# Performance work log

Hardware: AMD Instinct MI355X
Metric: run time of the kernel (lower is better)

Reference implementation:

```python
import jax, jax.numpy as jnp
import numpy as np

BLOCKS = 16
TEMP = 0.7
SINK_ITERS = 8
CUT = 8
GUMBEL_EPS = 1e-6
IN_EPS = 1e-5
NEG = -1e9  # stands in for log(0) = -inf; exp(NEG) == 0 in fp32, avoids nan grads


def setup_inputs() -> dict:
    key = jax.random.key(0)
    k1, k2, k3 = jax.random.split(key, 3)
    shape = (8, 512, 4096, 1)  # [B, C, H, W=1]
    return {
        "q": jax.random.normal(k1, shape, jnp.float32),
        "k": jax.random.normal(k2, shape, jnp.float32),
        "v": jax.random.normal(k3, shape, jnp.float32),
    }


def _block_cat(x, blocks):
    # torch: cat(x.chunk(blocks, dim=2)[:-1], dim=-1)
    # [B,C,H,W] -> [B,C,H/blocks,(blocks-1)*W]
    B, C, H, W = x.shape
    Hb = H // blocks
    xb = x.reshape(B, C, blocks, Hb, W)[:, :, : blocks - 1]  # drop last chunk
    return jnp.transpose(xb, (0, 1, 3, 2, 4)).reshape(B, C, Hb, (blocks - 1) * W)


def reference(q, k, v):
    B, C, H, W = q.shape
    Hb = H // BLOCKS
    N = BLOCKS - 1  # number of retained blocks

    b_q = _block_cat(q, BLOCKS)  # [B,C,Hb,N]
    b_k = _block_cat(k, BLOCKS)
    b_v = _block_cat(v, BLOCKS)

    # ---- AttentionPermMatrix: Gumbel-Sinkhorn soft permutation [B,N,N] ----
    sq = jnp.swapaxes(b_q.mean(axis=1), 1, 2)  # [B,N,Hb]
    sk = jnp.swapaxes(b_k.mean(axis=1), 1, 2)
    R = jnp.einsum('bie,bje->bij', sq, sk) * (C ** -0.5)  # [B,N,N]
    Rp = jax.nn.relu(R)
    pos = R > 0
    r = jnp.where(pos, jnp.log(jnp.where(pos, Rp, 1.0)), NEG)  # safe log(relu(R))
    u = jax.random.uniform(jax.random.key(42), r.shape, r.dtype)
    gumbel = -jnp.log(-jnp.log(u + GUMBEL_EPS) + GUMBEL_EPS)
    r = (r + gumbel) / TEMP
    for _ in range(SINK_ITERS):
        r = r - jax.nn.logsumexp(r, axis=2, keepdims=True)
        r = r - jax.nn.logsumexp(r, axis=1, keepdims=True)
    perm = jnp.exp(r)  # [B,N,N]

    # ---- permute blocks of k/v (perm broadcast over channel dim C) ----
    k_sort = jnp.einsum('bchn,bnm->bchm', b_k, perm)  # [B,C,Hb,N]
    v_sort = jnp.einsum('bchn,bnm->bchm', b_v, perm)

    # ---- cut: first CUT size-1 chunks along last dim, cat along dim=-2, transpose(1,3)
    def cut(x):
        # [B,C,Hb,N] -> [B,C,CUT*Hb,1] (chunk j occupies rows j*Hb:(j+1)*Hb) -> [B,1,CUT*Hb,C]
        xc = jnp.transpose(x[..., :CUT], (0, 1, 3, 2)).reshape(B, C, CUT * Hb, 1)
        return jnp.transpose(xc, (0, 3, 2, 1))

    k_cut = cut(k_sort)  # [B,1,M,C], M = CUT*Hb
    v_cut = cut(v_sort)
    q_t = jnp.transpose(q, (0, 3, 2, 1))  # [B,1,H,C]

    logits = jnp.einsum('bwhc,bwmc->bwhm', q_t, k_cut) / TEMP  # [B,1,H,M]
    attn = jax.nn.softmax(logits, axis=-1)
    val = jnp.einsum('bwhm,bwmc->bwhc', attn, v_cut)  # [B,1,H,C]

    # InstanceNorm2d (affine=False): normalize over spatial dims (2,3) per (B, channel)
    mu = val.mean(axis=(2, 3), keepdims=True)
    var = val.var(axis=(2, 3), keepdims=True)
    return (val - mu) / jnp.sqrt(var + IN_EPS)
```

## Files before the change

kernel.cpp:

```cpp
#include <hip/hip_runtime.h>
#include <stdint.h>

typedef _Float16 half_t;
typedef _Float16 half4 __attribute__((ext_vector_type(4)));
typedef _Float16 half8 __attribute__((ext_vector_type(8)));
typedef float floatx4 __attribute__((ext_vector_type(4)));

#define B_ 8
#define C_ 512
#define H_ 4096
#define HB 256
#define NB 15
#define CUT_ 8
#define M_ 2048
#define INV_TEMP (1.0f/0.7f)
#define NEG (-1e9f)

#define KROW 528
#define KT_BYTES 33792u
#define VT_BYTES 32768u

#define SQ_OFFB   0u
#define SK_OFFB   122880u
#define ST_OFFB   245760u
#define PERM_OFFB 245824u
#define KC16_OFFB 262144u
#define VC16_OFFB (262144u + 17301504u)
#define WS_NEED   (262144u + 17301504u + 16777216u)

__device__ __forceinline__ unsigned rotl32(unsigned x, unsigned n) {
    return (x << n) | (x >> (32u - n));
}
__device__ __forceinline__ void threefry2x32(unsigned k0, unsigned k1,
                                             unsigned x0, unsigned x1,
                                             unsigned &o0, unsigned &o1) {
    unsigned k2 = 0x1BD11BDAu ^ k0 ^ k1;
    x0 += k0; x1 += k1;
    x0+=x1; x1=rotl32(x1,13); x1^=x0;
    x0+=x1; x1=rotl32(x1,15); x1^=x0;
    x0+=x1; x1=rotl32(x1,26); x1^=x0;
    x0+=x1; x1=rotl32(x1, 6); x1^=x0;
    x0+=k1; x1+=k2+1u;
    x0+=x1; x1=rotl32(x1,17); x1^=x0;
    x0+=x1; x1=rotl32(x1,29); x1^=x0;
    x0+=x1; x1=rotl32(x1,16); x1^=x0;
    x0+=x1; x1=rotl32(x1,24); x1^=x0;
    x0+=k2; x1+=k0+2u;
    x0+=x1; x1=rotl32(x1,13); x1^=x0;
    x0+=x1; x1=rotl32(x1,15); x1^=x0;
    x0+=x1; x1=rotl32(x1,26); x1^=x0;
    x0+=x1; x1=rotl32(x1, 6); x1^=x0;
    x0+=k0; x1+=k1+3u;
    x0+=x1; x1=rotl32(x1,17); x1^=x0;
    x0+=x1; x1=rotl32(x1,29); x1^=x0;
    x0+=x1; x1=rotl32(x1,16); x1^=x0;
    x0+=x1; x1=rotl32(x1,24); x1^=x0;
    x0+=k1; x1+=k2+4u;
    x0+=x1; x1=rotl32(x1,13); x1^=x0;
    x0+=x1; x1=rotl32(x1,15); x1^=x0;
    x0+=x1; x1=rotl32(x1,26); x1^=x0;
    x0+=x1; x1=rotl32(x1, 6); x1^=x0;
    x0+=k2; x1+=k0+5u;
    o0 = x0; o1 = x1;
}

__device__ __forceinline__ void stage_tile8(const char* gsrc, char* lbase,
                                            int w, int lane, int nchunk) {
    #pragma unroll
    for (int i = 0; i < 5; i++) {
        int cc = w + 8*i;
        if (cc < nchunk) {
            __builtin_amdgcn_global_load_lds(
                (const __attribute__((address_space(1))) void*)(uintptr_t)
                    (gsrc + (size_t)cc*1024u + (size_t)lane*16u),
                (__attribute__((address_space(3))) void*)(uintptr_t)
                    (lbase + (size_t)cc*1024u),
                16, 0, 0);
        }
    }
}

__global__ void colmean_kernel(const float* __restrict__ q, const float* __restrict__ k,
                               float* __restrict__ sq, float* __restrict__ sk) {
    int id  = blockIdx.x * 256 + threadIdx.x;
    int h   = id % 3840;
    int rest= id / 3840;
    int b   = rest % 8;
    int seg = rest / 8;
    int c0  = seg * 64;
    const float* qb = q + ((size_t)b*C_ + c0) * H_ + h;
    const float* kb = k + ((size_t)b*C_ + c0) * H_ + h;
    float aq = 0.f, ak = 0.f;
    #pragma unroll 8
    for (int c = 0; c < 64; c++) {
        aq += qb[(size_t)c * H_];
        ak += kb[(size_t)c * H_];
    }
    atomicAdd(&sq[b*3840 + h], aq * (1.0f/512.0f));
    atomicAdd(&sk[b*3840 + h], ak * (1.0f/512.0f));
}

__global__ void perm_kernel(const float* __restrict__ sqg, const float* __restrict__ skg,
                            float* __restrict__ perm) {
    int b = blockIdx.x;
    int tid = threadIdx.x;
    __shared__ float sqs[NB*HB];
    __shared__ float sks[NB*HB];
    __shared__ float mat[NB][16];
    __shared__ float lse[NB];
    for (int i = tid; i < NB*HB; i += 256) {
        sqs[i] = sqg[b*3840 + i];
        sks[i] = skg[b*3840 + i];
    }
    __syncthreads();
    int i = tid / 15, j = tid % 15;
    if (tid < 225) {
        float acc = 0.f;
        for (int h = 0; h < HB; h++) acc += sqs[i*HB + h] * sks[j*HB + h];
        float R = acc * 0.044194173824159216f;
        float r0 = (R > 0.0f) ? logf(R) : NEG;
        int g = (b*15 + i)*15 + j;
        unsigned o0, o1;
        threefry2x32(0u, 42u, 0u, (unsigned)g, o0, o1);
        unsigned bits = o0 ^ o1;
        float u = __uint_as_float((bits >> 9) | 0x3f800000u) - 1.0f;
        float gum = -logf(-logf(u + 1e-6f) + 1e-6f);
        mat[i][j] = (r0 + gum) * INV_TEMP;
    }
    __syncthreads();
    for (int it = 0; it < 8; it++) {
        if (tid < 15) {
            float m = -3.4e38f;
            for (int jj = 0; jj < 15; jj++) m = fmaxf(m, mat[tid][jj]);
            float s = 0.f;
            for (int jj = 0; jj < 15; jj++) s += expf(mat[tid][jj] - m);
            lse[tid] = m + logf(s);
        }
        __syncthreads();
        if (tid < 225) mat[i][j] -= lse[i];
        __syncthreads();
        if (tid < 15) {
            float m = -3.4e38f;
            for (int ii = 0; ii < 15; ii++) m = fmaxf(m, mat[ii][tid]);
            float s = 0.f;
            for (int ii = 0; ii < 15; ii++) s += expf(mat[ii][tid] - m);
            lse[tid] = m + logf(s);
        }
        __syncthreads();
        if (tid < 225) mat[i][j] -= lse[j];
        __syncthreads();
    }
    if (tid < 225) perm[b*225 + tid] = expf(mat[i][j]);
}

__global__ __launch_bounds__(256)
void kcut_kernel(const float* __restrict__ k, const float* __restrict__ perm,
                 half_t* __restrict__ kc) {
    int bid  = blockIdx.x;
    int ct   = bid & 7;
    int chalf= (bid >> 3) & 1;
    int hch  = (bid >> 4) & 7;
    int b    = bid >> 7;
    int h0 = hch * 32;
    int tid = threadIdx.x;
    __shared__ float kt[32*481];
    __shared__ float pl[NB][CUT_];
    if (tid < NB*CUT_) pl[tid/CUT_][tid%CUT_] = perm[b*225 + (tid/CUT_)*15 + (tid%CUT_)];
    int cp = tid & 31;
    int hg = tid >> 5;
    int c0 = chalf*256 + ct*32;
    for (int it = 0; it < 15; it++) {
        int slot = tid + it*256;
        int h4 = slot & 7;
        int n  = (slot >> 3) % 15;
        int cc = slot / 120;
        float4 vv = *(const float4*)&k[((size_t)(b*C_ + c0 + cc))*H_ + n*HB + h0 + h4*4];
        *(float4*)&kt[cc*481 + n*32 + h4*4] = vv;
    }
    __syncthreads();
    float acc[CUT_][4];
    #pragma unroll
    for (int j = 0; j < CUT_; j++) { acc[j][0]=0.f; acc[j][1]=0.f; acc[j][2]=0.f; acc[j][3]=0.f; }
    #pragma unroll
    for (int n = 0; n < NB; n++) {
        float kv0 = kt[cp*481 + n*32 + hg*4 + 0];
        float kv1 = kt[cp*481 + n*32 + hg*4 + 1];
        float kv2 = kt[cp*481 + n*32 + hg*4 + 2];
        float kv3 = kt[cp*481 + n*32 + hg*4 + 3];
        #pragma unroll
        for (int j = 0; j < CUT_; j++) {
            float p = pl[n][j];
            acc[j][0] += kv0*p; acc[j][1] += kv1*p; acc[j][2] += kv2*p; acc[j][3] += kv3*p;
        }
    }
    int cs = c0 + (cp ^ (8*(hg & 3)));
    #pragma unroll
    for (int j = 0; j < CUT_; j++)
        for (int q2 = 0; q2 < 4; q2++) {
            int m = j*HB + h0 + hg*4 + q2;
            kc[(((size_t)b*64 + (m>>5))*32 + (m&31))*KROW + cs] = (half_t)acc[j][q2];
        }
}

__global__ __launch_bounds__(256)
void vcut_kernel(const float* __restrict__ v, const float* __restrict__ perm,
                 half_t* __restrict__ vc) {
    int bc = blockIdx.x;
    int b = bc >> 9;
    int c = bc & 511;
    int h = threadIdx.x;
    __shared__ float pl[NB][CUT_];
    if (h < NB*CUT_) pl[h/CUT_][h%CUT_] = perm[b*225 + (h/CUT_)*15 + (h%CUT_)];
    __syncthreads();
    const float* vb = v + (size_t)bc * H_ + h;
    float av[CUT_] = {0,0,0,0,0,0,0,0};
    #pragma unroll
    for (int n = 0; n < NB; n++) {
        float vv = vb[n*HB];
        #pragma unroll
        for (int j = 0; j < CUT_; j++) av[j] += vv * pl[n][j];
    }
    #pragma unroll
    for (int j = 0; j < CUT_; j++)
        vc[(((size_t)b*64 + j*8 + (h>>5))*512 + c)*32 + (h&31)] = (half_t)av[j];
}

__global__ __launch_bounds__(512, 2)
void attn_kernel(const float* __restrict__ q, const half_t* __restrict__ kc,
                 const half_t* __restrict__ vc, float* __restrict__ out,
                 float* __restrict__ stats) {
    __shared__ half_t ktile[2][32][KROW];
    __shared__ float  spart[2][64][36];
    __shared__ half_t pslab[2][64][40];
    __shared__ float  redbuf[8][2];

    int bid = blockIdx.x;
    int b   = bid & 7;
    int h0  = (bid >> 3) * 64;
    int tid = threadIdx.x;
    int w    = tid >> 6;
    int lane = tid & 63;
    int lm   = lane & 15;
    int quad = lane >> 4;
    int wm = w & 3;
    int wc = w >> 2;
    int row = 16*wm + lm;
    int key0 = 4*quad;
    int sxk = 8*((lm >> 2) & 3);

    const char* kbytes = (const char*)kc + (size_t)b * 64u * KT_BYTES;
    const char* vbytes = (const char*)vc + (size_t)b * 64u * VT_BYTES;

    stage_tile8(kbytes, (char*)&ktile[0][0][0], w, lane, 33);

    float (*qstage)[68] = reinterpret_cast<float(*)[68]>(&spart[0][0][0]);

    half8 qhi[8], qlo[8];
    for (int ch = 0; ch < 8; ch++) {
        int c0 = ch * 64;
        asm volatile("s_waitcnt lgkmcnt(0)\n\ts_barrier" ::: "memory");
        #pragma unroll
        for (int it = 0; it < 2; it++) {
            int slot = tid + it*512;
            int cc = slot >> 4;
            int h4 = slot & 15;
            float4 qv = *(const float4*)&q[((size_t)(b*C_ + c0 + cc))*H_ + h0 + h4*4];
            qstage[h4*4+0][cc] = qv.x;
            qstage[h4*4+1][cc] = qv.y;
            qstage[h4*4+2][cc] = qv.z;
            qstage[h4*4+3][cc] = qv.w;
        }
        asm volatile("s_waitcnt lgkmcnt(0)\n\ts_barrier" ::: "memory");
        if ((ch >> 2) == wc) {
            #pragma unroll
            for (int kk = 0; kk < 2; kk++) {
                int kb = (ch & 3)*2 + kk;
                const float* qp = &qstage[row][kk*32 + quad*8];
                float4 a = *(const float4*)qp;
                float4 c4 = *(const float4*)(qp + 4);
                float vals[8] = {a.x,a.y,a.z,a.w,c4.x,c4.y,c4.z,c4.w};
                half8 hh, hl;
                #pragma unroll
                for (int j = 0; j < 8; j++) {
                    float xv = vals[j] * INV_TEMP;
                    half_t h1 = (half_t)xv;
                    hh[j] = h1;
                    hl[j] = (half_t)(xv - (float)h1);
                }
                qhi[kb] = hh; qlo[kb] = hl;
            }
        }
    }

    floatx4 O[16];
    #pragma unroll
    for (int n = 0; n < 16; n++) O[n] = (floatx4)0.f;
    floatx4 Ol = (floatx4)0.f;
    float ms = -3.4e38f;
    half8 vone;
    #pragma unroll
    for (int j = 0; j < 8; j++) vone[j] = (half_t)1.0f;

    int buf = 0;
    for (int t = 0; t < 64; t++) {
        __syncthreads();
        half8 vreg[16];
        {
            const half_t* vt = (const half_t*)(vbytes + (size_t)t*VT_BYTES);
            #pragma unroll
            for (int n = 0; n < 16; n++)
                vreg[n] = *(const half8*)(vt + (256*wc + 16*n + lm)*32 + quad*8);
        }
        if (t + 1 < 64)
            stage_tile8(kbytes + (size_t)(t+1)*KT_BYTES, (char*)&ktile[buf^1][0][0], w, lane, 33);

        floatx4 acc0 = (floatx4)0.f, acc1 = (floatx4)0.f;
        __builtin_amdgcn_s_setprio(1);
        #pragma unroll
        for (int kb = 0; kb < 8; kb++) {
            int coff = (256*wc + 32*kb + quad*8) ^ sxk;
            half8 a0 = *(const half8*)&ktile[buf][lm][coff];
            half8 a1 = *(const half8*)&ktile[buf][16 + lm][coff];
            acc0 = __builtin_amdgcn_mfma_f32_16x16x32_f16(a0, qhi[kb], acc0, 0, 0, 0);
            acc0 = __builtin_amdgcn_mfma_f32_16x16x32_f16(a0, qlo[kb], acc0, 0, 0, 0);
            acc1 = __builtin_amdgcn_mfma_f32_16x16x32_f16(a1, qhi[kb], acc1, 0, 0, 0);
            acc1 = __builtin_amdgcn_mfma_f32_16x16x32_f16(a1, qlo[kb], acc1, 0, 0, 0);
        }
        __builtin_amdgcn_s_setprio(0);
        *(floatx4*)&spart[wc][row][key0]      = acc0;
        *(floatx4*)&spart[wc][row][16 + key0] = acc1;
        asm volatile("s_waitcnt lgkmcnt(0)\n\ts_barrier" ::: "memory");

        floatx4 pp0 = *(const floatx4*)&spart[wc^1][row][key0];
        floatx4 pp1 = *(const floatx4*)&spart[wc^1][row][16 + key0];
        float s0[4], s1[4];
        #pragma unroll
        for (int r = 0; r < 4; r++) {
            s0[r] = acc0[r] + pp0[r];
            s1[r] = acc1[r] + pp1[r];
        }
        float m2 = fmaxf(fmaxf(fmaxf(s0[0],s0[1]), fmaxf(s0[2],s0[3])),
                         fmaxf(fmaxf(s1[0],s1[1]), fmaxf(s1[2],s1[3])));
        m2 = fmaxf(m2, __shfl_xor(m2, 16, 64));
        m2 = fmaxf(m2, __shfl_xor(m2, 32, 64));
        int need = (m2 > ms + 8.0f) ? 1 : 0;
        if (__any(need)) {
            float mn = fmaxf(ms, m2);
            float aown = __expf(ms - mn);
            ms = mn;
            float ar[4];
            #pragma unroll
            for (int r = 0; r < 4; r++) ar[r] = __shfl(aown, key0 + r, 64);
            #pragma unroll
            for (int r = 0; r < 4; r++) Ol[r] *= ar[r];
            #pragma unroll
            for (int n = 0; n < 16; n++) {
                #pragma unroll
                for (int r = 0; r < 4; r++) O[n][r] *= ar[r];
            }
        }
        half4 hp0, hp1;
        #pragma unroll
        for (int r = 0; r < 4; r++) {
            hp0[r] = (half_t)__expf(s0[r] - ms);
            hp1[r] = (half_t)__expf(s1[r] - ms);
        }
        *(half4*)&pslab[wc][row][key0]      = hp0;
        *(half4*)&pslab[wc][row][16 + key0] = hp1;
        half8 pa = *(const half8*)&pslab[wc][row][quad*8];
        __builtin_amdgcn_s_setprio(1);
        #pragma unroll
        for (int n = 0; n < 16; n++)
            O[n] = __builtin_amdgcn_mfma_f32_16x16x32_f16(pa, vreg[n], O[n], 0, 0, 0);
        Ol = __builtin_amdgcn_mfma_f32_16x16x32_f16(pa, vone, Ol, 0, 0, 0);
        __builtin_amdgcn_s_setprio(0);
        buf ^= 1;
    }

    float inv4[4];
    #pragma unroll
    for (int r = 0; r < 4; r++) inv4[r] = 1.0f / Ol[r];
    float sa = 0.f, sb = 0.f;
    int rowg = h0 + 16*wm + quad*4;
    #pragma unroll
    for (int n = 0; n < 16; n++) {
        #pragma unroll
        for (int r = 0; r < 4; r++) {
            float o = O[n][r] * inv4[r];
            out[((size_t)b*H_ + rowg + r)*C_ + 256*wc + 16*n + lm] = o;
            sa += o; sb += o*o;
        }
    }
    #pragma unroll
    for (int msk = 1; msk < 64; msk <<= 1) {
        sa += __shfl_xor(sa, msk, 64);
        sb += __shfl_xor(sb, msk, 64);
    }
    if (lane == 0) { redbuf[w][0] = sa; redbuf[w][1] = sb; }
    __syncthreads();
    if (tid == 0) {
        float a = 0.f, c2 = 0.f;
        for (int w2 = 0; w2 < 8; w2++) { a += redbuf[w2][0]; c2 += redbuf[w2][1]; }
        atomicAdd(&stats[b*2    ], a);
        atomicAdd(&stats[b*2 + 1], c2);
    }
}

__global__ void norm_kernel(float* __restrict__ out, const float* __restrict__ stats) {
    size_t i = (size_t)blockIdx.x * 256 + threadIdx.x;
    int b = (int)(i >> 19);
    float4 vv = ((float4*)out)[i];
    const float inv = 1.0f / (4096.0f * 512.0f);
    float mu  = stats[b*2] * inv;
    float var = stats[b*2 + 1] * inv - mu*mu;
    float rs  = rsqrtf(var + 1e-5f);
    vv.x = (vv.x - mu) * rs;
    vv.y = (vv.y - mu) * rs;
    vv.z = (vv.z - mu) * rs;
    vv.w = (vv.w - mu) * rs;
    ((float4*)out)[i] = vv;
}

extern "C" void kernel_launch(void* const* d_in, const int* in_sizes, int n_in,
                              void* d_out, int out_size, void* d_ws, size_t ws_size,
                              hipStream_t stream) {
    const float* q = (const float*)d_in[0];
    const float* k = (const float*)d_in[1];
    const float* v = (const float*)d_in[2];
    float* out = (float*)d_out;
    if (ws_size < (size_t)WS_NEED) return;

    float*  sq    = (float*) ((char*)d_ws + SQ_OFFB);
    float*  sk    = (float*) ((char*)d_ws + SK_OFFB);
    float*  stats = (float*) ((char*)d_ws + ST_OFFB);
    float*  perm  = (float*) ((char*)d_ws + PERM_OFFB);
    half_t* kc    = (half_t*)((char*)d_ws + KC16_OFFB);
    half_t* vc    = (half_t*)((char*)d_ws + VC16_OFFB);

    hipMemsetAsync(d_ws, 0, (size_t)KC16_OFFB, stream);

    colmean_kernel<<<960,  256, 0, stream>>>(q, k, sq, sk);
    perm_kernel   <<<8,    256, 0, stream>>>(sq, sk, perm);
    kcut_kernel   <<<1024, 256, 0, stream>>>(k, perm, kc);
    vcut_kernel   <<<4096, 256, 0, stream>>>(v, perm, vc);
    attn_kernel   <<<512,  512, 0, stream>>>(q, kc, vc, out, stats);
    norm_kernel   <<<16384,256, 0, stream>>>(out, stats);
}
```

Measured before the change: 653.9 us.

## Vectorize colmean loads and stage V tiles through LDS in attention

The column-mean kernel now has each thread handle four adjacent positions with float4 loads, cutting the grid fourfold while keeping the same number of atomics in total. In the attention kernel, each thread now loads one contiguous 64-byte row of the V tile into registers and writes it to a new padded LDS tile after the QK MFMAs. The PV MFMAs then read their operands from LDS instead of doing scattered per-fragment global loads. This adds about 40KB of shared memory per block and extra LDS traffic, which may affect occupancy at two blocks per CU.

```diff
diff --git a/kernel.cpp b/kernel.cpp
--- a/kernel.cpp
+++ b/kernel.cpp
@@ -83,21 +83,29 @@
 __global__ void colmean_kernel(const float* __restrict__ q, const float* __restrict__ k,
                                float* __restrict__ sq, float* __restrict__ sk) {
     int id  = blockIdx.x * 256 + threadIdx.x;
-    int h   = id % 3840;
-    int rest= id / 3840;
-    int b   = rest % 8;
-    int seg = rest / 8;
-    int c0  = seg * 64;
-    const float* qb = q + ((size_t)b*C_ + c0) * H_ + h;
-    const float* kb = k + ((size_t)b*C_ + c0) * H_ + h;
-    float aq = 0.f, ak = 0.f;
+    int h4  = id % 960;
+    int rest= id / 960;
+    int b   = rest & 7;
+    int c0  = (rest >> 3) * 64;
+    const float* qb = q + ((size_t)b*C_ + c0) * H_ + h4*4;
+    const float* kb = k + ((size_t)b*C_ + c0) * H_ + h4*4;
+    float4 aq = {0.f,0.f,0.f,0.f}, ak = {0.f,0.f,0.f,0.f};
     #pragma unroll 8
     for (int c = 0; c < 64; c++) {
-        aq += qb[(size_t)c * H_];
-        ak += kb[(size_t)c * H_];
-    }
-    atomicAdd(&sq[b*3840 + h], aq * (1.0f/512.0f));
-    atomicAdd(&sk[b*3840 + h], ak * (1.0f/512.0f));
+        float4 qv = *(const float4*)&qb[(size_t)c * H_];
+        float4 kv = *(const float4*)&kb[(size_t)c * H_];
+        aq.x += qv.x; aq.y += qv.y; aq.z += qv.z; aq.w += qv.w;
+        ak.x += kv.x; ak.y += kv.y; ak.z += kv.z; ak.w += kv.w;
+    }
+    int base = b*3840 + h4*4;
+    atomicAdd(&sq[base+0], aq.x * (1.0f/512.0f));
+    atomicAdd(&sq[base+1], aq.y * (1.0f/512.0f));
+    atomicAdd(&sq[base+2], aq.z * (1.0f/512.0f));
+    atomicAdd(&sq[base+3], aq.w * (1.0f/512.0f));
+    atomicAdd(&sk[base+0], ak.x * (1.0f/512.0f));
+    atomicAdd(&sk[base+1], ak.y * (1.0f/512.0f));
+    atomicAdd(&sk[base+2], ak.z * (1.0f/512.0f));
+    atomicAdd(&sk[base+3], ak.w * (1.0f/512.0f));
 }
 
 __global__ void perm_kernel(const float* __restrict__ sqg, const float* __restrict__ skg,
@@ -230,6 +238,7 @@
                  const half_t* __restrict__ vc, float* __restrict__ out,
                  float* __restrict__ stats) {
     __shared__ half_t ktile[2][32][KROW];
+    __shared__ half_t vtile[512][40];
     __shared__ float  spart[2][64][36];
     __shared__ half_t pslab[2][64][40];
     __shared__ float  redbuf[8][2];
@@ -304,12 +313,11 @@
     int buf = 0;
     for (int t = 0; t < 64; t++) {
         __syncthreads();
-        half8 vreg[16];
+        float4 vst[4];
         {
             const half_t* vt = (const half_t*)(vbytes + (size_t)t*VT_BYTES);
             #pragma unroll
-            for (int n = 0; n < 16; n++)
-                vreg[n] = *(const half8*)(vt + (256*wc + 16*n + lm)*32 + quad*8);
+            for (int i = 0; i < 4; i++) vst[i] = *(const float4*)(vt + tid*32 + i*8);
         }
         if (t + 1 < 64)
             stage_tile8(kbytes + (size_t)(t+1)*KT_BYTES, (char*)&ktile[buf^1][0][0], w, lane, 33);
@@ -327,6 +335,8 @@
             acc1 = __builtin_amdgcn_mfma_f32_16x16x32_f16(a1, qlo[kb], acc1, 0, 0, 0);
         }
         __builtin_amdgcn_s_setprio(0);
+        #pragma unroll
+        for (int i = 0; i < 4; i++) *(float4*)&vtile[tid][i*8] = vst[i];
         *(floatx4*)&spart[wc][row][key0]      = acc0;
         *(floatx4*)&spart[wc][row][16 + key0] = acc1;
         asm volatile("s_waitcnt lgkmcnt(0)\n\ts_barrier" ::: "memory");
@@ -370,8 +380,10 @@
         half8 pa = *(const half8*)&pslab[wc][row][quad*8];
         __builtin_amdgcn_s_setprio(1);
         #pragma unroll
-        for (int n = 0; n < 16; n++)
-            O[n] = __builtin_amdgcn_mfma_f32_16x16x32_f16(pa, vreg[n], O[n], 0, 0, 0);
+        for (int n = 0; n < 16; n++) {
+            half8 vb = *(const half8*)&vtile[256*wc + 16*n + lm][quad*8];
+            O[n] = __builtin_amdgcn_mfma_f32_16x16x32_f16(pa, vb, O[n], 0, 0, 0);
+        }
         Ol = __builtin_amdgcn_mfma_f32_16x16x32_f16(pa, vone, Ol, 0, 0, 0);
         __builtin_amdgcn_s_setprio(0);
         buf ^= 1;
@@ -439,7 +451,7 @@
 
     hipMemsetAsync(d_ws, 0, (size_t)KC16_OFFB, stream);
 
-    colmean_kernel<<<960,  256, 0, stream>>>(q, k, sq, sk);
+    colmean_kernel<<<240,  256, 0, stream>>>(q, k, sq, sk);
     perm_kernel   <<<8,    256, 0, stream>>>(sq, sk, perm);
     kcut_kernel   <<<1024, 256, 0, stream>>>(k, perm, kc);
     vcut_kernel   <<<4096, 256, 0, stream>>>(v, perm, vc);
```

New measurement: 570.1 us. -12.8%, faster.
